# Kernel optimization log

Hardware: AMD Instinct MI355X
Metric: run time of the kernel (lower is better)

## Reference

```python
import jax, jax.numpy as jnp
import numpy as np

B, L, H = 8, 1024, 512
CHUNK = 16  # query-row chunk size for the score computation; L % CHUNK == 0


def setup_inputs() -> dict:
    key = jax.random.key(0)
    ks = jax.random.split(key, 6)
    s = 1.0 / np.sqrt(H)  # torch nn.Linear default init bound
    return {
        "inputs": jax.random.normal(ks[0], (B, L, H), jnp.float32),
        "W1": jax.random.uniform(ks[1], (H, H), jnp.float32, -s, s),
        "b1": jax.random.uniform(ks[2], (H,), jnp.float32, -s, s),
        "W2": jax.random.uniform(ks[3], (H, H), jnp.float32, -s, s),
        "b2": jax.random.uniform(ks[4], (H,), jnp.float32, -s, s),
        # torch: nn.init.normal_(q, mean=-0.02, std=0.02)
        "q": jax.random.normal(ks[5], (H,), jnp.float32) * 0.02 - 0.02,
    }


def _scores(u1, u2, q):
    # u[b,i,j] = tanh(u1[b,i,:] + u2[b,j,:]) . q  -- computed in row-chunks to
    # avoid materializing the full [B,L,L,H] tensor the torch loop implies.
    Bx, Lx, Hx = u1.shape
    n = Lx // CHUNK
    u1c = u1.reshape(Bx, n, CHUNK, Hx).transpose(1, 0, 2, 3)  # [n, B, c, H]

    def step(carry, u1_i):
        t = jnp.tanh(u1_i[:, :, None, :] + u2[:, None, :, :])  # [B, c, L, H]
        return carry, jnp.einsum('bclh,h->bcl', t, q)

    _, s = jax.lax.scan(jax.checkpoint(step), None, u1c)  # [n, B, c, L]
    return s.transpose(1, 0, 2, 3).reshape(Bx, Lx, Lx)


def reference(inputs, W1, b1, W2, b2, q):
    u1 = inputs @ W1.T + b1  # [B, L, H]
    u2 = inputs @ W2.T + b2  # [B, L, H]
    u = _scores(u1, u2, q)   # [B, L, L]
    # relu=False in init, so no relu on u
    a = jax.nn.softmax(u, axis=2)
    h = jnp.einsum('bij,bjh->bih', a, inputs)  # [B, L, H]
    return h, a
```

## Files before the change

### kernel.cpp

```cpp
#include <hip/hip_runtime.h>

typedef _Float16 f16;
typedef _Float16 f16x2 __attribute__((ext_vector_type(2)));
typedef _Float16 f16x4 __attribute__((ext_vector_type(4)));
typedef _Float16 f16x8 __attribute__((ext_vector_type(8)));
typedef float f32x4 __attribute__((ext_vector_type(4)));

#define LOG2E_X2 2.8853900817779268f

__constant__ float D8[8] = {0.543915f, 0.177997f, 0.0652351f, 0.0242575f,
                            0.00903807f, 0.00336823f, 0.00125536f, 0.000467884f};

static __device__ __forceinline__ void gl2lds16(const void* g, void* l) {
  __builtin_amdgcn_global_load_lds((const __attribute__((address_space(1))) void*)g,
                                   (__attribute__((address_space(3))) void*)l, 16, 0, 0);
}


__global__ __launch_bounds__(256) void k_prep_x(const float* __restrict__ X,
                                                f16* __restrict__ Xh, f16* __restrict__ XhT) {
  const int ht = blockIdx.x, it = blockIdx.y, b = blockIdx.z;
  __shared__ f16 Lt[64][72];
  const int t = threadIdx.x;
  const int r = t >> 4, c4 = (t & 15) * 4;
  const float* Xb = X + ((size_t)b * 1024 + it * 64) * 512 + ht * 64;
#pragma unroll
  for (int k = 0; k < 4; ++k) {
    const int rr = r + 16 * k;
    float4 v = *(const float4*)&Xb[(size_t)rr * 512 + c4];
    f16 h0 = (f16)v.x, h1 = (f16)v.y, h2 = (f16)v.z, h3 = (f16)v.w;
    *(f16x4*)&Xh[((size_t)b * 1024 + it * 64 + rr) * 512 + ht * 64 + c4] = {h0, h1, h2, h3};
    Lt[c4 + 0][rr] = h0; Lt[c4 + 1][rr] = h1; Lt[c4 + 2][rr] = h2; Lt[c4 + 3][rr] = h3;
  }
  __syncthreads();
  const int hr = t >> 2, seg = t & 3;
  f16* dst = &XhT[((size_t)b * 512 + ht * 64 + hr) * 1024 + it * 64 + seg * 16];
  *(f16x8*)(dst) = *(const f16x8*)&Lt[hr][seg * 16];
  *(f16x8*)(dst + 8) = *(const f16x8*)&Lt[hr][seg * 16 + 8];
}

__global__ __launch_bounds__(256) void k_prep_w(const float* __restrict__ W1,
                                                const float* __restrict__ W2,
                                                f16* __restrict__ Wh) {
  const int row = blockIdx.x, z = blockIdx.y, t = threadIdx.x;
  const float* W = z ? W2 : W1;
  float2 v = *(const float2*)&W[(size_t)row * 512 + t * 2];
  *(f16x2*)&Wh[(size_t)z * 262144 + (size_t)row * 512 + t * 2] = {(f16)v.x, (f16)v.y};
}

__global__ void k_prep_b(const float* __restrict__ b1, const float* __restrict__ b2,
                         float* __restrict__ biasCat) {
  const int t = blockIdx.x * 256 + threadIdx.x;
  biasCat[t] = t < 512 ? b1[t] : b2[t - 512];
}

template <int NM>
__global__ __launch_bounds__(256) void k_trig(const float* __restrict__ u,
                                              const float* __restrict__ q,
                                              f16* __restrict__ At, f16* __restrict__ Bt,
                                              float* __restrict__ qa, float* __restrict__ qb,
                                              int m0, int wq) {
  const int i = blockIdx.x, t = threadIdx.x;
  const float w = 0.62831853f;
  const float2 a2 = *(const float2*)&u[(size_t)i * 1024 + 2 * t];
  const float2 b2 = *(const float2*)&u[(size_t)i * 1024 + 512 + 2 * t];
  const float2 q2 = *(const float2*)&q[2 * t];
  if (wq) {
    float sa = q2.x * a2.x + q2.y * a2.y;
    float sb = q2.x * b2.x + q2.y * b2.y;
#pragma unroll
    for (int o = 1; o < 64; o <<= 1) { sa += __shfl_xor(sa, o); sb += __shfl_xor(sb, o); }
    __shared__ float red[8];
    const int lane = t & 63, widx = t >> 6;
    if (lane == 0) { red[widx] = sa; red[4 + widx] = sb; }
    __syncthreads();
    if (t == 0) qa[i] = red[0] + red[1] + red[2] + red[3];
    if (t == 1) qb[i] = red[4] + red[5] + red[6] + red[7];
  }
  float s1[4], c1[4], sm_[4], cm_[4];
  const float ang[4] = {w * a2.x, w * a2.y, w * b2.x, w * b2.y};
#pragma unroll
  for (int uu = 0; uu < 4; ++uu) {
    __sincosf(ang[uu], &s1[uu], &c1[uu]);
    if (m0 == 1) { sm_[uu] = s1[uu]; cm_[uu] = c1[uu]; }
    else __sincosf(m0 * ang[uu], &sm_[uu], &cm_[uu]);
  }
  const size_t ldT = (size_t)NM * 1024;
  f16* Ar = At + (size_t)i * ldT + 2 * t;
  f16* Br = Bt + (size_t)i * ldT + 2 * t;
#pragma unroll
  for (int j = 0; j < NM; ++j) {
    const float dm = D8[m0 - 1 + j];
    const float qdx = q2.x * dm, qdy = q2.y * dm;
    *(f16x2*)(Ar + j * 1024)       = {(f16)(qdx * sm_[0]), (f16)(qdy * sm_[1])};
    *(f16x2*)(Ar + j * 1024 + 512) = {(f16)(qdx * cm_[0]), (f16)(qdy * cm_[1])};
    *(f16x2*)(Br + j * 1024)       = {(f16)cm_[2], (f16)cm_[3]};
    *(f16x2*)(Br + j * 1024 + 512) = {(f16)sm_[2], (f16)sm_[3]};
    if (j + 1 < NM) {
#pragma unroll
      for (int uu = 0; uu < 4; ++uu) {
        const float ns = sm_[uu] * c1[uu] + cm_[uu] * s1[uu];
        const float nc = cm_[uu] * c1[uu] - sm_[uu] * s1[uu];
        sm_[uu] = ns; cm_[uu] = nc;
      }
    }
  }
}

template <int MODE, int ACC, int T, int WR, int WC, int FI, int FJ>
__global__ __launch_bounds__(T, 2) void k_gemmG(
    const f16* __restrict__ A, const f16* __restrict__ B, float* __restrict__ C,
    const float* __restrict__ bias0, int Kloop, int ldAB, long halfA, long halfC) {
  constexpr int BM = WR * FI * 16;
  constexpr int BN = WC * FJ * 16;
  __shared__ alignas(16) char smA[2][BM * 128];
  __shared__ alignas(16) char smB[2][BN * 128];
  const int t = threadIdx.x;
  const int nx = blockIdx.x, my = blockIdx.y, z = blockIdx.z;
  const f16* Ab; const f16* Bb; float* Cb; const float* bias = nullptr;
  int ldC;
  if (MODE == 0) {
    Ab = A + (size_t)my * BM * ldAB;
    Bb = B + (size_t)nx * BN * ldAB;
    Cb = C + (size_t)my * BM * 1024 + nx * BN;
    bias = bias0 + nx * BN;
    ldC = 1024;
  } else if (MODE == 1) {
    const int b = z & 7, h = z >> 3;
    Ab = A + ((size_t)(b * 1024 + my * BM)) * ldAB + h * halfA;
    Bb = B + ((size_t)(b * 1024 + nx * BN)) * ldAB + h * halfA;
    Cb = C + h * halfC + ((size_t)(b * 1024 + my * BM)) * 1024 + nx * BN;
    ldC = 1024;
  } else {
    Ab = A + (size_t)z * 1048576 + (size_t)my * BM * ldAB;
    Bb = B + (size_t)z * 524288 + (size_t)nx * BN * ldAB;
    Cb = C + (size_t)z * 524288 + (size_t)my * BM * 512 + nx * BN;
    ldC = 512;
  }
  const int wid = t >> 6, lane = t & 63;
  const int wr = wid / WC, wc = wid % WC;
  const int rl = lane & 15, kc = lane >> 4;
  f32x4 acc[FI][FJ] = {};

  auto stage = [&](int buf, int kt) {
    const f16* gA = Ab + kt * 64;
    const f16* gB = Bb + kt * 64;
    constexpr int LA = BM * 8 / T, LB = BN * 8 / T;
#pragma unroll
    for (int ii = 0; ii < LA; ++ii) {
      const int idx = ii * T + t;
      const int row = idx >> 3, c = idx & 7;
      gl2lds16(gA + (size_t)row * ldAB + ((c ^ (row & 7)) * 8),
               smA[buf] + ii * (T * 16) + wid * 1024);
    }
#pragma unroll
    for (int ii = 0; ii < LB; ++ii) {
      const int idx = ii * T + t;
      const int row = idx >> 3, c = idx & 7;
      gl2lds16(gB + (size_t)row * ldAB + ((c ^ (row & 7)) * 8),
               smB[buf] + ii * (T * 16) + wid * 1024);
    }
  };

  const int nkt = Kloop >> 6;
  stage(0, 0);
  __syncthreads();
  for (int kt = 0; kt < nkt; ++kt) {
    const int cur = kt & 1;
    if (kt + 1 < nkt) stage(cur ^ 1, kt + 1);
    const char* lA = smA[cur];
    const char* lB = smB[cur];
#pragma unroll
    for (int kk = 0; kk < 2; ++kk) {
      f16x8 av[FI], bv[FJ];
#pragma unroll
      for (int fi = 0; fi < FI; ++fi) {
        const int rloc = (wr * FI + fi) * 16 + rl;
        av[fi] = *(const f16x8*)(lA + rloc * 128 + (((kc + 4 * kk) ^ (rloc & 7)) << 4));
      }
#pragma unroll
      for (int fj = 0; fj < FJ; ++fj) {
        const int cloc = (wc * FJ + fj) * 16 + rl;
        bv[fj] = *(const f16x8*)(lB + cloc * 128 + (((kc + 4 * kk) ^ (cloc & 7)) << 4));
      }
#pragma unroll
      for (int fi = 0; fi < FI; ++fi)
#pragma unroll
        for (int fj = 0; fj < FJ; ++fj)
          acc[fi][fj] = __builtin_amdgcn_mfma_f32_16x16x32_f16(av[fi], bv[fj], acc[fi][fj], 0, 0, 0);
    }
    __syncthreads();
  }

#pragma unroll
  for (int fj = 0; fj < FJ; ++fj) {
    const int gcol = (wc * FJ + fj) * 16 + rl;
    const float bvv = (MODE == 0) ? bias[gcol] : 0.f;
#pragma unroll
    for (int fi = 0; fi < FI; ++fi) {
      const int grow0 = (wr * FI + fi) * 16 + kc * 4;
      f32x4 v = acc[fi][fj];
#pragma unroll
      for (int r = 0; r < 4; ++r) {
        const size_t o = (size_t)(grow0 + r) * ldC + gcol;
        float x = v[r] + bvv;
        if (ACC) x += Cb[o];
        Cb[o] = x;
      }
    }
  }
}

__global__ __launch_bounds__(256) void k_softmax2(const float* __restrict__ P0,
                                                  const float* __restrict__ P1,
                                                  const float* __restrict__ qa,
                                                  const float* __restrict__ qb,
                                                  float* __restrict__ out_a,
                                                  f16* __restrict__ a16) {
  const int row = blockIdx.x, t = threadIdx.x;
  const int b = row >> 10;
  const size_t off = (size_t)row * 1024 + t * 4;
  float4 p0 = *(const float4*)(P0 + off);
  float4 p1 = *(const float4*)(P1 + off);
  float4 qb4 = *(const float4*)(qb + (size_t)b * 1024 + t * 4);
  const float qi = qa[row];
  float4 v;
  v.x = p0.x + p1.x + 0.2f * (qi + qb4.x);
  v.y = p0.y + p1.y + 0.2f * (qi + qb4.y);
  v.z = p0.z + p1.z + 0.2f * (qi + qb4.z);
  v.w = p0.w + p1.w + 0.2f * (qi + qb4.w);
  float m = fmaxf(fmaxf(v.x, v.y), fmaxf(v.z, v.w));
#pragma unroll
  for (int o = 1; o < 64; o <<= 1) m = fmaxf(m, __shfl_xor(m, o));
  __shared__ float red[4];
  const int w = t >> 6, ln = t & 63;
  if (ln == 0) red[w] = m;
  __syncthreads();
  m = fmaxf(fmaxf(red[0], red[1]), fmaxf(red[2], red[3]));
  v.x = __expf(v.x - m); v.y = __expf(v.y - m);
  v.z = __expf(v.z - m); v.w = __expf(v.w - m);
  float s = v.x + v.y + v.z + v.w;
#pragma unroll
  for (int o = 1; o < 64; o <<= 1) s += __shfl_xor(s, o);
  __syncthreads();
  if (ln == 0) red[w] = s;
  __syncthreads();
  s = red[0] + red[1] + red[2] + red[3];
  const float inv = 1.0f / s;
  v.x *= inv; v.y *= inv; v.z *= inv; v.w *= inv;
  *(float4*)(out_a + off) = v;
  *(f16x4*)(a16 + off) = {(f16)v.x, (f16)v.y, (f16)v.z, (f16)v.w};
}

typedef short s16x2 __attribute__((ext_vector_type(2)));

static __device__ __forceinline__ float fdot2f(f16x2 a, f16x2 b, float c) {
#if __has_builtin(__builtin_amdgcn_fdot2)
  return __builtin_amdgcn_fdot2(a, b, c, false);
#else
  return c + (float)a[0] * (float)b[0] + (float)a[1] * (float)b[1];
#endif
}

__global__ void k_qprep(const float* __restrict__ q, f16* __restrict__ qh,
                        float* __restrict__ qsum) {
  const int t = threadIdx.x;
  float v = q[t];
  qh[t] = (f16)v;
  float s = v;
#pragma unroll
  for (int o = 1; o < 64; o <<= 1) s += __shfl_xor(s, o);
  __shared__ float red[8];
  if ((t & 63) == 0) red[t >> 6] = s;
  __syncthreads();
  if (t == 0) {
    float tot = 0.f;
#pragma unroll
    for (int i = 0; i < 8; ++i) tot += red[i];
    *qsum = tot;
  }
}

__global__ __launch_bounds__(256) void k_gemm_exp(
    const float* __restrict__ X, const float* __restrict__ W1,
    const float* __restrict__ b1, const float* __restrict__ W2,
    const float* __restrict__ b2, f16* __restrict__ e1, f16* __restrict__ e2) {
  const int z = blockIdx.z;
  const float* W = z ? W2 : W1;
  const float* bias = z ? b2 : b1;
  f16* out = z ? e2 : e1;
  const int r0 = blockIdx.y * 64;
  const int c0 = blockIdx.x * 64;
  __shared__ alignas(16) float Xs[64][68];
  __shared__ alignas(16) float Ws[64][68];
  const int t = threadIdx.x;
  const int row = t >> 2, seg = t & 3;
  const int tr = t >> 4, tc = t & 15;
  float acc[4][4] = {};
#pragma unroll 1
  for (int k0 = 0; k0 < 512; k0 += 64) {
    const float4* gx = (const float4*)(X + (size_t)(r0 + row) * 512 + k0 + seg * 16);
    float4* lx = (float4*)(&Xs[row][seg * 16]);
    lx[0] = gx[0]; lx[1] = gx[1]; lx[2] = gx[2]; lx[3] = gx[3];
    const float4* gw = (const float4*)(W + (size_t)(c0 + row) * 512 + k0 + seg * 16);
    float4* lw = (float4*)(&Ws[row][seg * 16]);
    lw[0] = gw[0]; lw[1] = gw[1]; lw[2] = gw[2]; lw[3] = gw[3];
    __syncthreads();
#pragma unroll 4
    for (int kk = 0; kk < 64; kk += 4) {
      float4 av[4], bv[4];
#pragma unroll
      for (int ii = 0; ii < 4; ++ii) av[ii] = *(const float4*)&Xs[tr + 16 * ii][kk];
#pragma unroll
      for (int jj = 0; jj < 4; ++jj) bv[jj] = *(const float4*)&Ws[tc + 16 * jj][kk];
#pragma unroll
      for (int ii = 0; ii < 4; ++ii) {
#pragma unroll
        for (int jj = 0; jj < 4; ++jj) {
          acc[ii][jj] = fmaf(av[ii].x, bv[jj].x, acc[ii][jj]);
          acc[ii][jj] = fmaf(av[ii].y, bv[jj].y, acc[ii][jj]);
          acc[ii][jj] = fmaf(av[ii].z, bv[jj].z, acc[ii][jj]);
          acc[ii][jj] = fmaf(av[ii].w, bv[jj].w, acc[ii][jj]);
        }
      }
    }
    __syncthreads();
  }
#pragma unroll
  for (int ii = 0; ii < 4; ++ii) {
    const int r = r0 + tr + 16 * ii;
#pragma unroll
    for (int jj = 0; jj < 4; ++jj) {
      const int c = c0 + tc + 16 * jj;
      float u = acc[ii][jj] + bias[c];
      float val = u * LOG2E_X2 - 4.0f;
      val = fminf(6.6759f, fmaxf(-14.6759f, val));
      out[(size_t)r * 512 + c] = (f16)exp2f(val);
    }
  }
}

template <int P>
static __device__ __forceinline__ void tanh_dot_step(const f16x8 (&Av)[4],
                                                     const f16x8 (&Bv)[4],
                                                     const f16x8& Qv, float (&acc)[4][4],
                                                     int c256, int kmag, int two2) {
  f16x2 qp = __builtin_shufflevector(Qv, Qv, 2 * P, 2 * P + 1);
#pragma unroll
  for (int jj = 0; jj < 4; ++jj) {
    f16x2 bp = __builtin_shufflevector(Bv[jj], Bv[jj], 2 * P, 2 * P + 1);
#pragma unroll
    for (int ii = 0; ii < 4; ++ii) {
      f16x2 ap = __builtin_shufflevector(Av[ii], Av[ii], 2 * P, 2 * P + 1);
      f16x2 d, r, tt;
      asm("v_pk_fma_f16 %0, %3, %4, %5\n\t"
          "v_pk_sub_i16 %1, %6, %0\n\t"
          "v_pk_fma_f16 %2, %0, %1, %7 neg_lo:[1,0,0] neg_hi:[1,0,0]\n\t"
          "v_pk_mul_f16 %1, %1, %2\n\t"
          "v_pk_fma_f16 %2, %0, %1, %7 neg_lo:[1,0,0] neg_hi:[1,0,0]\n\t"
          "v_pk_mul_f16 %1, %1, %2"
          : "=&v"(d), "=&v"(r), "=&v"(tt)
          : "v"(ap), "v"(bp), "v"(c256), "v"(kmag), "v"(two2));
      acc[ii][jj] = fdot2f(r, qp, acc[ii][jj]);
    }
  }
}

__global__ __launch_bounds__(256) void k_scores(const f16* __restrict__ e1,
                                                const f16* __restrict__ e2,
                                                const f16* __restrict__ qh,
                                                const float* __restrict__ qsum_p,
                                                float* __restrict__ out_a) {
  const int b = blockIdx.z, it = blockIdx.y, jt = blockIdx.x;
  __shared__ alignas(16) f16 As[64][72];
  __shared__ alignas(16) f16 Bs[64][72];
  __shared__ alignas(16) f16 Qs[512];
  const int t = threadIdx.x;
  const size_t eA = (size_t)(b * 1024 + it * 64) * 512;
  const size_t eB = (size_t)(b * 1024 + jt * 64) * 512;
  if (t < 64) ((uint4*)Qs)[t] = ((const uint4*)qh)[t];
  const int row = t >> 2, seg = t & 3;
  const int tr = t >> 4, tc = t & 15;
  const int c256 = 0x1C001C00;
  const int kmag = 0x77987798;
  const int two2 = 0x40004000;
  float acc[4][4] = {};
#pragma unroll 1
  for (int h0 = 0; h0 < 512; h0 += 64) {
    const f16* gA = e1 + eA + (size_t)row * 512 + h0;
    const f16* gB = e2 + eB + (size_t)row * 512 + h0;
    *(uint4*)(&As[row][seg * 8]) = *(const uint4*)(gA + seg * 8);
    *(uint4*)(&As[row][seg * 8 + 32]) = *(const uint4*)(gA + seg * 8 + 32);
    *(uint4*)(&Bs[row][seg * 8]) = *(const uint4*)(gB + seg * 8);
    *(uint4*)(&Bs[row][seg * 8 + 32]) = *(const uint4*)(gB + seg * 8 + 32);
    __syncthreads();
#pragma unroll 2
    for (int g = 0; g < 8; ++g) {
      f16x8 Av[4], Bv[4], Qv;
#pragma unroll
      for (int ii = 0; ii < 4; ++ii) Av[ii] = *(const f16x8*)&As[tr + 16 * ii][g * 8];
#pragma unroll
      for (int jj = 0; jj < 4; ++jj) Bv[jj] = *(const f16x8*)&Bs[tc + 16 * jj][g * 8];
      Qv = *(const f16x8*)&Qs[h0 + g * 8];
      tanh_dot_step<0>(Av, Bv, Qv, acc, c256, kmag, two2);
      tanh_dot_step<1>(Av, Bv, Qv, acc, c256, kmag, two2);
      tanh_dot_step<2>(Av, Bv, Qv, acc, c256, kmag, two2);
      tanh_dot_step<3>(Av, Bv, Qv, acc, c256, kmag, two2);
    }
    __syncthreads();
  }
  const float qs = *qsum_p;
#pragma unroll
  for (int ii = 0; ii < 4; ++ii) {
    const size_t orow = (size_t)(b * 1024 + it * 64 + tr + 16 * ii) * 1024;
#pragma unroll
    for (int jj = 0; jj < 4; ++jj)
      out_a[orow + jt * 64 + tc + 16 * jj] = qs - acc[ii][jj] * (1.0f / 128.0f);
  }
}

__global__ __launch_bounds__(256) void k_softmax(float* __restrict__ a) {
  float* row = a + (size_t)blockIdx.x * 1024;
  const int t = threadIdx.x;
  float4 v = ((const float4*)row)[t];
  float m = fmaxf(fmaxf(v.x, v.y), fmaxf(v.z, v.w));
#pragma unroll
  for (int o = 1; o < 64; o <<= 1) m = fmaxf(m, __shfl_xor(m, o));
  __shared__ float red[4];
  const int w = t >> 6, ln = t & 63;
  if (ln == 0) red[w] = m;
  __syncthreads();
  m = fmaxf(fmaxf(red[0], red[1]), fmaxf(red[2], red[3]));
  v.x = __expf(v.x - m); v.y = __expf(v.y - m);
  v.z = __expf(v.z - m); v.w = __expf(v.w - m);
  float s = v.x + v.y + v.z + v.w;
#pragma unroll
  for (int o = 1; o < 64; o <<= 1) s += __shfl_xor(s, o);
  __syncthreads();
  if (ln == 0) red[w] = s;
  __syncthreads();
  s = red[0] + red[1] + red[2] + red[3];
  const float inv = 1.0f / s;
  v.x *= inv; v.y *= inv; v.z *= inv; v.w *= inv;
  ((float4*)row)[t] = v;
}

__global__ __launch_bounds__(256) void k_av(const float* __restrict__ a,
                                            const float* __restrict__ X,
                                            float* __restrict__ h) {
  const int b = blockIdx.z;
  const int i0 = blockIdx.y * 64;
  const int c0 = blockIdx.x * 64;
  __shared__ alignas(16) float As[64][68];
  __shared__ alignas(16) float Xs[64][68];
  const float* Ab = a + (size_t)b * 1024 * 1024;
  const float* Xb = X + (size_t)b * 1024 * 512;
  const int t = threadIdx.x;
  const int row = t >> 2, seg = t & 3;
  const int tr = t >> 4, tc = t & 15;
  float acc[4][4] = {};
#pragma unroll 1
  for (int k0 = 0; k0 < 1024; k0 += 64) {
    const float4* ga = (const float4*)(Ab + (size_t)(i0 + row) * 1024 + k0 + seg * 16);
    float4* la = (float4*)(&As[row][seg * 16]);
    la[0] = ga[0]; la[1] = ga[1]; la[2] = ga[2]; la[3] = ga[3];
    const float4* gx = (const float4*)(Xb + (size_t)(k0 + row) * 512 + c0 + seg * 16);
    float4* lx = (float4*)(&Xs[row][seg * 16]);
    lx[0] = gx[0]; lx[1] = gx[1]; lx[2] = gx[2]; lx[3] = gx[3];
    __syncthreads();
#pragma unroll 8
    for (int k = 0; k < 64; ++k) {
      float av[4], bv[4];
#pragma unroll
      for (int ii = 0; ii < 4; ++ii) av[ii] = As[tr + 16 * ii][k];
#pragma unroll
      for (int jj = 0; jj < 4; ++jj) bv[jj] = Xs[k][tc + 16 * jj];
#pragma unroll
      for (int ii = 0; ii < 4; ++ii) {
#pragma unroll
        for (int jj = 0; jj < 4; ++jj)
          acc[ii][jj] = fmaf(av[ii], bv[jj], acc[ii][jj]);
      }
    }
    __syncthreads();
  }
#pragma unroll
  for (int ii = 0; ii < 4; ++ii) {
    const size_t orow = (size_t)b * 1024 * 512 + (size_t)(i0 + tr + 16 * ii) * 512;
#pragma unroll
    for (int jj = 0; jj < 4; ++jj)
      h[orow + c0 + tc + 16 * jj] = acc[ii][jj];
  }
}

extern "C" void kernel_launch(void* const* d_in, const int* in_sizes, int n_in,
                              void* d_out, int out_size, void* d_ws, size_t ws_size,
                              hipStream_t stream) {
  const float* inputs = (const float*)d_in[0];
  const float* W1 = (const float*)d_in[1];
  const float* b1 = (const float*)d_in[2];
  const float* W2 = (const float*)d_in[3];
  const float* b2 = (const float*)d_in[4];
  const float* q = (const float*)d_in[5];

  float* out_h = (float*)d_out;
  float* out_a = out_h + 4194304;

  const size_t FIXED = 101781504ULL;
  const size_t PER_M = 33554432ULL;
  if (ws_size < FIXED + PER_M) {
    char* ws = (char*)d_ws;
    f16* e1 = (f16*)ws;
    f16* e2 = (f16*)(ws + 8388608);
    f16* qh = (f16*)(ws + 16777216);
    float* qsum = (float*)(ws + 16778240);
    k_qprep<<<1, 512, 0, stream>>>(q, qh, qsum);
    k_gemm_exp<<<dim3(8, 128, 2), 256, 0, stream>>>(inputs, W1, b1, W2, b2, e1, e2);
    k_scores<<<dim3(16, 16, 8), 256, 0, stream>>>(e1, e2, qh, qsum, out_a);
    k_softmax<<<8192, 256, 0, stream>>>(out_a);
    k_av<<<dim3(8, 16, 8), 256, 0, stream>>>(out_a, inputs, out_h);
    return;
  }

  int nm = 8;
  while (FIXED + (size_t)nm * PER_M > ws_size) nm >>= 1;

  char* p = (char*)d_ws;
  f16* Xh = (f16*)p;            p += 8388608;
  f16* XhT = (f16*)p;           p += 8388608;
  f16* Wh = (f16*)p;            p += 1048576;
  f16* a16 = (f16*)p;           p += 16777216;
  float* qa = (float*)p;        p += 32768;
  float* qb = (float*)p;        p += 32768;
  float* biasCat = (float*)p;   p += 4096;
  float* P0 = (float*)p;        p += 33554432;
  float* P1 = (float*)p;        p += 33554432;
  f16* At = (f16*)p;            p += (size_t)nm * 16777216;
  f16* Bt = (f16*)p;

  float* u = out_a;

  k_prep_x<<<dim3(8, 16, 8), 256, 0, stream>>>(inputs, Xh, XhT);
  k_prep_w<<<dim3(512, 2), 256, 0, stream>>>(W1, W2, Wh);
  k_prep_b<<<4, 256, 0, stream>>>(b1, b2, biasCat);
  k_gemmG<0, 0, 512, 2, 4, 4, 4><<<dim3(4, 64, 1), 512, 0, stream>>>(
      Xh, Wh, u, biasCat, 512, 512, 0, 0);

  const int chunks = 8 / nm;
  for (int cch = 0; cch < chunks; ++cch) {
    const int m0 = cch * nm + 1;
    switch (nm) {
      case 8: k_trig<8><<<8192, 256, 0, stream>>>(u, q, At, Bt, qa, qb, m0, cch == 0); break;
      case 4: k_trig<4><<<8192, 256, 0, stream>>>(u, q, At, Bt, qa, qb, m0, cch == 0); break;
      case 2: k_trig<2><<<8192, 256, 0, stream>>>(u, q, At, Bt, qa, qb, m0, cch == 0); break;
      default: k_trig<1><<<8192, 256, 0, stream>>>(u, q, At, Bt, qa, qb, m0, cch == 0); break;
    }
    const int Kloop = nm * 512;
    const int ldAB = nm * 1024;
    const long halfA = (long)nm * 512;
    if (cch == 0)
      k_gemmG<1, 0, 512, 2, 4, 8, 4><<<dim3(4, 4, 16), 512, 0, stream>>>(
          At, Bt, P0, nullptr, Kloop, ldAB, halfA, 8388608L);
    else
      k_gemmG<1, 1, 512, 2, 4, 8, 4><<<dim3(4, 4, 16), 512, 0, stream>>>(
          At, Bt, P0, nullptr, Kloop, ldAB, halfA, 8388608L);
  }

  k_softmax2<<<8192, 256, 0, stream>>>(P0, P1, qa, qb, out_a, a16);
  k_gemmG<2, 0, 256, 2, 2, 4, 4><<<dim3(4, 8, 8), 256, 0, stream>>>(
      a16, XhT, out_h, nullptr, 1024, 1024, 0, 0);
}
```

Before: 307.9 us.

## Add dedicated 128x128 GEMM with K=32 tiles for score matmul

Replaces the generic MODE 1 GEMM, which used 256x256 tiles with 512 threads, with a specialized kernel for the trig-feature score GEMM. The new kernel uses 128x128 tiles, 256 threads, K-steps of 32 with swizzled LDS and the 16x16x32 MFMA, and launch bounds allowing 4 blocks per CU. This gives 1024 blocks instead of 256, aiming for better CU occupancy and load balance. The cost is lower data reuse per tile and more synchronisation steps along K.

```diff
diff --git a/kernel.cpp b/kernel.cpp
--- a/kernel.cpp
+++ b/kernel.cpp
@@ -107,6 +107,81 @@
   }
 }
 
+template <int ACC>
+__global__ __launch_bounds__(256, 4) void k_gemm32(
+    const f16* __restrict__ A, const f16* __restrict__ B, float* __restrict__ C,
+    int Kloop, int ldAB, long halfA, long halfC) {
+  __shared__ alignas(16) char smA[2][8192];
+  __shared__ alignas(16) char smB[2][8192];
+  const int t = threadIdx.x;
+  const int nx = blockIdx.x, my = blockIdx.y, z = blockIdx.z;
+  const int b = z & 7, h = z >> 3;
+  const f16* Ab = A + ((size_t)(b * 1024 + my * 128)) * ldAB + h * halfA;
+  const f16* Bb = B + ((size_t)(b * 1024 + nx * 128)) * ldAB + h * halfA;
+  float* Cb = C + h * halfC + ((size_t)(b * 1024 + my * 128)) * 1024 + nx * 128;
+  const int wid = t >> 6, lane = t & 63;
+  const int wr = wid >> 1, wc = wid & 1;
+  const int rl = lane & 15, kc = lane >> 4;
+  f32x4 acc[4][4] = {};
+
+  auto stage = [&](int buf, int kt) {
+    const f16* gA = Ab + kt * 32;
+    const f16* gB = Bb + kt * 32;
+#pragma unroll
+    for (int ii = 0; ii < 2; ++ii) {
+      const int idx = ii * 256 + t;
+      const int row = idx >> 2, sp = idx & 3;
+      const int sl = sp ^ ((row ^ (row >> 2)) & 3);
+      gl2lds16(gA + (size_t)row * ldAB + sl * 8, smA[buf] + ii * 4096 + wid * 1024);
+      gl2lds16(gB + (size_t)row * ldAB + sl * 8, smB[buf] + ii * 4096 + wid * 1024);
+    }
+  };
+
+  const int nkt = Kloop >> 5;
+  stage(0, 0);
+  __syncthreads();
+  for (int kt = 0; kt < nkt; ++kt) {
+    const int cur = kt & 1;
+    if (kt + 1 < nkt) stage(cur ^ 1, kt + 1);
+    const char* lA = smA[cur];
+    const char* lB = smB[cur];
+    f16x8 av[4], bv[4];
+#pragma unroll
+    for (int fi = 0; fi < 4; ++fi) {
+      const int r = wr * 64 + fi * 16 + rl;
+      av[fi] = *(const f16x8*)(lA + r * 64 + ((kc ^ ((r ^ (r >> 2)) & 3)) << 4));
+    }
+#pragma unroll
+    for (int fj = 0; fj < 4; ++fj) {
+      const int c = wc * 64 + fj * 16 + rl;
+      bv[fj] = *(const f16x8*)(lB + c * 64 + ((kc ^ ((c ^ (c >> 2)) & 3)) << 4));
+    }
+#pragma unroll
+    for (int fi = 0; fi < 4; ++fi)
+#pragma unroll
+      for (int fj = 0; fj < 4; ++fj)
+        acc[fi][fj] = __builtin_amdgcn_mfma_f32_16x16x32_f16(av[fi], bv[fj], acc[fi][fj], 0, 0, 0);
+    __syncthreads();
+  }
+
+#pragma unroll
+  for (int fj = 0; fj < 4; ++fj) {
+    const int gcol = wc * 64 + fj * 16 + rl;
+#pragma unroll
+    for (int fi = 0; fi < 4; ++fi) {
+      const int grow0 = wr * 64 + fi * 16 + kc * 4;
+      f32x4 v = acc[fi][fj];
+#pragma unroll
+      for (int r = 0; r < 4; ++r) {
+        const size_t o = (size_t)(grow0 + r) * 1024 + gcol;
+        float x = v[r];
+        if (ACC) x += Cb[o];
+        Cb[o] = x;
+      }
+    }
+  }
+}
+
 template <int MODE, int ACC, int T, int WR, int WC, int FI, int FJ>
 __global__ __launch_bounds__(T, 2) void k_gemmG(
     const f16* __restrict__ A, const f16* __restrict__ B, float* __restrict__ C,
@@ -124,12 +199,6 @@
     Bb = B + (size_t)nx * BN * ldAB;
     Cb = C + (size_t)my * BM * 1024 + nx * BN;
     bias = bias0 + nx * BN;
-    ldC = 1024;
-  } else if (MODE == 1) {
-    const int b = z & 7, h = z >> 3;
-    Ab = A + ((size_t)(b * 1024 + my * BM)) * ldAB + h * halfA;
-    Bb = B + ((size_t)(b * 1024 + nx * BN)) * ldAB + h * halfA;
-    Cb = C + h * halfC + ((size_t)(b * 1024 + my * BM)) * 1024 + nx * BN;
     ldC = 1024;
   } else {
     Ab = A + (size_t)z * 1048576 + (size_t)my * BM * ldAB;
@@ -559,11 +628,9 @@
     const int ldAB = nm * 1024;
     const long halfA = (long)nm * 512;
     if (cch == 0)
-      k_gemmG<1, 0, 512, 2, 4, 8, 4><<<dim3(4, 4, 16), 512, 0, stream>>>(
-          At, Bt, P0, nullptr, Kloop, ldAB, halfA, 8388608L);
+      k_gemm32<0><<<dim3(8, 8, 16), 256, 0, stream>>>(At, Bt, P0, Kloop, ldAB, halfA, 8388608L);
     else
-      k_gemmG<1, 1, 512, 2, 4, 8, 4><<<dim3(4, 4, 16), 512, 0, stream>>>(
-          At, Bt, P0, nullptr, Kloop, ldAB, halfA, 8388608L);
+      k_gemm32<1><<<dim3(8, 8, 16), 256, 0, stream>>>(At, Bt, P0, Kloop, ldAB, halfA, 8388608L);
   }
 
   k_softmax2<<<8192, 256, 0, stream>>>(P0, P1, qa, qb, out_a, a16);
```

Result: slower. 419.6 us (+36.3%).
